# Performance work log

Hardware: AMD Instinct MI355X
Metric: run time of the kernel (lower is better)

Reference implementation:

```python
import jax, jax.numpy as jnp
import numpy as np

BETA = 0.5

def gelu(x):
    return jax.nn.gelu(x, approximate=False)  # torch F.gelu default is exact erf

def setup_inputs() -> dict:
    key = jax.random.key(0)
    ks = jax.random.split(key, 10)
    N, F, PH, P, D, H, C, E = 50000, 128, 64, 8, 4, 128, 10, 1600000
    s = 0.05
    return {
        "x": jax.random.normal(ks[0], (N, F), jnp.float32),
        "W_proj": jax.random.normal(ks[1], (PH, F), jnp.float32) * s,
        "b_proj": jnp.zeros((PH,), jnp.float32),
        "W_x": jax.random.normal(ks[2], (H, F), jnp.float32) * s,
        "b_x": jnp.zeros((H,), jnp.float32),
        "W_path": jax.random.normal(ks[3], (H, D * PH), jnp.float32) * s,
        "b_path": jnp.zeros((H,), jnp.float32),
        "W_A": jax.random.normal(ks[4], (H, N), jnp.float32) * s,
        "b_A": jnp.zeros((H,), jnp.float32),
        "W_end": jax.random.normal(ks[5], (C, H), jnp.float32) * s,
        "b_end": jnp.zeros((C,), jnp.float32),
        "index": jax.random.randint(ks[6], (N, P, D), 0, N, jnp.int64)
                 if jax.config.jax_enable_x64 else jax.random.randint(ks[6], (N, P, D), 0, N, jnp.int32),
        "edge_index": jax.random.randint(ks[7], (2, E), 0, N, jnp.int32),
    }

def reference(x, W_proj, b_proj, W_x, b_x, W_path, b_path, W_A, b_A, W_end, b_end, index, edge_index):
    N = x.shape[0]
    # path projection then per-node path gather: [N, P, D, PH]
    pp = x @ W_proj.T + b_proj
    path = pp[index]
    Np, P, D, PH = path.shape
    # node MLP (dropout off in eval)
    h = gelu(x @ W_x.T + b_x)  # [N, H]
    # concat path encoder: [N, P, D*PH] -> [N, P, H]
    pi = gelu(path.reshape(Np, P, D * PH) @ W_path.T + b_path)
    # dot-product path attention with softmax over path dim
    att = jax.nn.softmax(jnp.einsum('nh,nph->np', h, pi), axis=-1)
    path_agg = jnp.einsum('np,nph->nh', att, pi)
    # sparse adjacency (COO, weights=1) times Linear weight: A @ W_A.T + b_A
    M = W_A.T  # [N, H]
    A_x = jax.ops.segment_sum(M[edge_index[1]], edge_index[0], num_segments=N) + b_A
    out = (1.0 - BETA) * (path_agg + h) + BETA * A_x
    out = gelu(out)
    return out @ W_end.T + b_end
```

## Files before the change

### kernel.cpp

```cpp
#include <hip/hip_runtime.h>
#include <hip/hip_bf16.h>
#include <math.h>

#define NF   128
#define NPH  64
#define NP   8
#define ND   4
#define NH   128
#define NC   10
#define BCAP 2560

typedef __bf16 bf16;
typedef __attribute__((ext_vector_type(4))) __bf16 bf16x4;
typedef __attribute__((ext_vector_type(8))) __bf16 bf16x8;
typedef __attribute__((ext_vector_type(4))) float f32x4;

template<int CTRL>
__device__ __forceinline__ float dpp_add(float x) {
    int t = __builtin_amdgcn_update_dpp(0, __float_as_int(x), CTRL, 0xf, 0xf, false);
    return x + __int_as_float(t);
}
__device__ __forceinline__ float row16_sum(float x) {
    x = dpp_add<0x121>(x);
    x = dpp_add<0x122>(x);
    x = dpp_add<0x124>(x);
    x = dpp_add<0x128>(x);
    return x;
}

__device__ __forceinline__ float gelu_fast(float x) {
    float z = fabsf(x) * 0.70710678118654752f;
    float t = __builtin_amdgcn_rcpf(1.0f + 0.47047f * z);
    float poly = t * (0.3480242f + t * (-0.0958798f + t * 0.7478556f));
    float erfv = 1.0f - poly * __expf(-z * z);
    float s = copysignf(erfv, x);
    return 0.5f * x * (1.0f + s);
}

#define GLOAD_LDS16(g, l)                                                     \
    __builtin_amdgcn_global_load_lds(                                         \
        (const __attribute__((address_space(1))) unsigned int*)(g),           \
        (__attribute__((address_space(3))) unsigned int*)(l), 16, 0, 0)

__device__ __forceinline__ bf16x8 cvt8(float4 a, float4 b) {
    bf16x8 r;
    r[0] = (bf16)a.x; r[1] = (bf16)a.y; r[2] = (bf16)a.z; r[3] = (bf16)a.w;
    r[4] = (bf16)b.x; r[5] = (bf16)b.y; r[6] = (bf16)b.z; r[7] = (bf16)b.w;
    return r;
}

__device__ __forceinline__ void add8(float* a, uint4 v) {
    a[0] += __uint_as_float(v.x << 16);  a[1] += __uint_as_float(v.x & 0xffff0000u);
    a[2] += __uint_as_float(v.y << 16);  a[3] += __uint_as_float(v.y & 0xffff0000u);
    a[4] += __uint_as_float(v.z << 16);  a[5] += __uint_as_float(v.z & 0xffff0000u);
    a[6] += __uint_as_float(v.w << 16);  a[7] += __uint_as_float(v.w & 0xffff0000u);
}

__global__ __launch_bounds__(256) void k_front(
    const float* __restrict__ x,
    const float* __restrict__ Wproj, const float* __restrict__ bproj,
    const float* __restrict__ Wx,    const float* __restrict__ bx,
    bf16* __restrict__ pp, bf16* __restrict__ hb,
    const float* __restrict__ WA, bf16* __restrict__ Mb,
    const int* __restrict__ esrc, const int* __restrict__ edst,
    int* __restrict__ gcur, unsigned* __restrict__ pairs,
    int N, int E, int nbuck, int nbP, int nbT)
{
    __shared__ alignas(16) char smem[33280];
    const int tid = threadIdx.x;

    const int bid = blockIdx.x;
    const int two = 2 * nbP;
    int cls, idx;
    if (bid < two) { cls = bid & 1; idx = bid >> 1; }
    else           { cls = 1; idx = nbP + (bid - two); }

    if (cls == 0) {
        bf16* x_s = (bf16*)smem;
        const int w = tid >> 6, l = tid & 63;
        const int c = l & 15, g = l >> 4;

        bf16x8 bfr[3][4];
        float bias[3];
        #pragma unroll
        for (int t = 0; t < 3; ++t) {
            int ch = (w * 3 + t) * 16 + c;
            const float* wr = (ch < NPH) ? &Wproj[(size_t)ch * NF]
                                         : &Wx[(size_t)(ch - NPH) * NF];
            bias[t] = (ch < NPH) ? bproj[ch] : bx[ch - NPH];
            #pragma unroll
            for (int ks = 0; ks < 4; ++ks) {
                const float* src = wr + ks * 32 + g * 8;
                bfr[t][ks] = cvt8(*(const float4*)src, *(const float4*)(src + 4));
            }
        }

        const int n0 = idx * 64;
        #pragma unroll
        for (int rr = 0; rr < 8; ++rr) {
            int id  = rr * 256 + tid;
            int row = id >> 5, c4 = id & 31;
            float4 v = make_float4(0.f, 0.f, 0.f, 0.f);
            if (n0 + row < N) v = *(const float4*)&x[(size_t)(n0 + row) * NF + c4 * 4];
            bf16x4 o;
            o[0] = (bf16)v.x; o[1] = (bf16)v.y; o[2] = (bf16)v.z; o[3] = (bf16)v.w;
            *(bf16x4*)&x_s[row * 136 + c4 * 4] = o;
        }
        __syncthreads();

        f32x4 acc[4][3] = {};
        #pragma unroll
        for (int rt = 0; rt < 4; ++rt)
            #pragma unroll
            for (int ks = 0; ks < 4; ++ks) {
                bf16x8 a = *(const bf16x8*)&x_s[(rt * 16 + c) * 136 + ks * 32 + g * 8];
                #pragma unroll
                for (int t = 0; t < 3; ++t)
                    acc[rt][t] = __builtin_amdgcn_mfma_f32_16x16x32_bf16(
                        a, bfr[t][ks], acc[rt][t], 0, 0, 0);
            }

        #pragma unroll
        for (int rt = 0; rt < 4; ++rt) {
            #pragma unroll
            for (int t = 0; t < 3; ++t) {
                int ch = (w * 3 + t) * 16 + c;
                #pragma unroll
                for (int i = 0; i < 4; ++i) {
                    int n = n0 + rt * 16 + g * 4 + i;
                    if (n >= N) continue;
                    float v = acc[rt][t][i] + bias[t];
                    if (ch < NPH) pp[(size_t)n * NPH + ch] = (bf16)v;
                    else          hb[(size_t)n * NH + (ch - NPH)] = (bf16)gelu_fast(v);
                }
            }
        }
    } else if (idx < nbT) {
        float* tt = (float*)smem;
        const int n0 = idx * 64;
        const int w = tid >> 6, l = tid & 63;
        #pragma unroll
        for (int rep = 0; rep < 32; ++rep) {
            int hh = rep * 4 + w;
            int n  = n0 + l;
            tt[hh * 65 + l] = (n < N) ? WA[(size_t)hh * N + n] : 0.f;
        }
        __syncthreads();
        #pragma unroll
        for (int rep = 0; rep < 32; ++rep) {
            int n_l = rep * 2 + (tid >> 7);
            int n   = n0 + n_l;
            if (n < N) Mb[(size_t)n * NH + (tid & 127)] = (bf16)tt[(tid & 127) * 65 + n_l];
        }
    } else {
        int* cnt  = (int*)smem;
        int* bofs = cnt + 800;
        const int tile = (idx - nbT) * 4096;
        for (int i = tid; i < nbuck; i += 256) cnt[i] = 0;
        __syncthreads();
        #pragma unroll
        for (int k = 0; k < 16; ++k) {
            int i = tile + k * 256 + tid;
            if (i < E) atomicAdd(&cnt[esrc[i] >> 6], 1);
        }
        __syncthreads();
        for (int i = tid; i < nbuck; i += 256) {
            int c = cnt[i];
            bofs[i] = c ? atomicAdd(&gcur[i], c) : 0;
            cnt[i] = 0;
        }
        __syncthreads();
        #pragma unroll
        for (int k = 0; k < 16; ++k) {
            int i = tile + k * 256 + tid;
            if (i < E) {
                int s = esrc[i], b = s >> 6;
                int r = atomicAdd(&cnt[b], 1);
                pairs[(size_t)b * BCAP + bofs[b] + r] =
                    ((unsigned)(s & 63) << 16) | (unsigned)edst[i];
            }
        }
    }
}

__global__ __launch_bounds__(256, 3) void k_mid2(
    const unsigned* __restrict__ pairs, const int* __restrict__ gcur,
    const bf16* __restrict__ Mb, const float* __restrict__ bA,
    bf16* __restrict__ axbuf2,
    const bf16* __restrict__ pp, const bf16* __restrict__ hb,
    const float* __restrict__ Wpath, const float* __restrict__ bpath,
    const int* __restrict__ index, bf16* __restrict__ aggbuf,
    int N, int E, int nbuck, int nrounds)
{
    __shared__ alignas(16) char smem[35328];
    const int tid = threadIdx.x;

    const int bid = blockIdx.x;
    const int two = 2 * nbuck;
    int cls, idx;
    if (bid < two) { cls = bid & 1; idx = bid >> 1; }
    else           { cls = 0; idx = nbuck + (bid - two); }

    if (cls == 1) {
        int* hist  = (int*)smem;
        int* sc    = hist + 64;
        int* cur   = hist + 128;
        unsigned short* dstl = (unsigned short*)(smem + 768);
        const int b = idx, t = tid;
        const int cnt = gcur[b];
        const unsigned* pb = pairs + (size_t)b * BCAP;

        if (t < 64) hist[t] = 0;
        __syncthreads();
        for (int j = t; j < cnt; j += 256)
            atomicAdd(&hist[pb[j] >> 16], 1);
        __syncthreads();
        if (t < 64) sc[t] = hist[t];
        __syncthreads();
        for (int off = 1; off < 64; off <<= 1) {
            int u = (t < 64 && t >= off) ? sc[t - off] : 0;
            __syncthreads();
            if (t < 64) sc[t] += u;
            __syncthreads();
        }
        if (t < 64) cur[t] = sc[t] - hist[t];
        __syncthreads();
        for (int j = t; j < cnt; j += 256) {
            unsigned p = pb[j];
            int pos = atomicAdd(&cur[p >> 16], 1);
            dstl[pos] = (unsigned short)(p & 0xffffu);
        }
        __syncthreads();

        const int w = t >> 6, l = t & 63;
        const int e = l >> 4, q = l & 15;
        const unsigned short* Mu = (const unsigned short*)Mb;
        const int nb0 = b * 64;
        #pragma unroll 1
        for (int it = 0; it < 16; ++it) {
            const int node = it * 4 + w;
            const int n = nb0 + node;
            const int le = sc[node];
            int j = le - hist[node];
            float acc[8] = {0.f, 0.f, 0.f, 0.f, 0.f, 0.f, 0.f, 0.f};
            for (; j + 32 <= le; j += 32) {
                int d[8];
                #pragma unroll
                for (int k = 0; k < 8; ++k) d[k] = dstl[j + k * 4 + e];
                uint4 v[8];
                #pragma unroll
                for (int k = 0; k < 8; ++k)
                    v[k] = *((const uint4*)(Mu + (size_t)d[k] * NH) + q);
                #pragma unroll
                for (int k = 0; k < 8; ++k) add8(acc, v[k]);
            }
            for (; j + 4 <= le; j += 4) {
                int d0 = dstl[j + e];
                uint4 v0 = *((const uint4*)(Mu + (size_t)d0 * NH) + q);
                add8(acc, v0);
            }
            if (e < le - j) {
                int d0 = dstl[j + e];
                uint4 v0 = *((const uint4*)(Mu + (size_t)d0 * NH) + q);
                add8(acc, v0);
            }
            #pragma unroll
            for (int k = 0; k < 8; ++k) {
                acc[k] += __shfl_xor(acc[k], 16, 64);
                acc[k] += __shfl_xor(acc[k], 32, 64);
            }
            if (l < 16 && n < N) {
                float4 bA0 = *(const float4*)&bA[q * 8];
                float4 bA1 = *(const float4*)&bA[q * 8 + 4];
                bf16x8 o;
                o[0] = (bf16)(0.5f * (acc[0] + bA0.x));
                o[1] = (bf16)(0.5f * (acc[1] + bA0.y));
                o[2] = (bf16)(0.5f * (acc[2] + bA0.z));
                o[3] = (bf16)(0.5f * (acc[3] + bA0.w));
                o[4] = (bf16)(0.5f * (acc[4] + bA1.x));
                o[5] = (bf16)(0.5f * (acc[5] + bA1.y));
                o[6] = (bf16)(0.5f * (acc[6] + bA1.z));
                o[7] = (bf16)(0.5f * (acc[7] + bA1.w));
                *(bf16x8*)&axbuf2[(size_t)n * NH + q * 8] = o;
            }
        }
        return;
    }

    bf16*  path_s = (bf16*)smem;
    bf16*  h_sb   = (bf16*)(smem + 32768);
    float* s_red  = (float*)(smem + 34816);

    const int w   = tid >> 6;
    const int l   = tid & 63;
    const int c   = l & 15;
    const int g   = l >> 4;
    const int nl  = g >> 1;

    bf16x8 bfrag[2][8];
    #pragma unroll
    for (int ht = 0; ht < 2; ++ht) {
        int hg = (w * 2 + ht) * 16 + c;
        #pragma unroll
        for (int ks = 0; ks < 8; ++ks) {
            const float* src = &Wpath[(size_t)hg * 256 + ks * 32 + g * 8];
            bfrag[ht][ks] = cvt8(*(const float4*)src, *(const float4*)(src + 4));
        }
    }
    const float bp0 = bpath[(w * 2 + 0) * 16 + c];
    const float bp1 = bpath[(w * 2 + 1) * 16 + c];

    auto stage = [&](int round, int b) {
        const int n0 = round * 4;
        #pragma unroll
        for (int rr = 0; rr < 4; ++rr) {
            int id  = rr * 256 + tid;
            int row = id >> 5;
            int cc  = id & 31;
            int ls  = cc ^ (row & 7);
            int d   = ls >> 3, q = ls & 7;
            int nn  = row >> 3, p = row & 7;
            int idx2 = index[(size_t)(n0 + nn) * (NP * ND) + p * ND + d];
            GLOAD_LDS16(pp + (size_t)idx2 * NPH + q * 8, &path_s[b * 8192 + id * 8]);
        }
        if (tid < 64) {
            int node = tid >> 4, q = tid & 15;
            GLOAD_LDS16(hb + (size_t)(n0 + node) * NH + q * 8,
                        &h_sb[(b * 4 + node) * 128 + q * 8]);
        }
    };

    int r = idx;
    const int G = gridDim.x - nbuck;
    if (r < nrounds) stage(r, 0);
    int buf = 0;

    for (; r < nrounds; r += G) {
        const int n0 = r * 4;
        __syncthreads();
        if (r + G < nrounds) stage(r + G, buf ^ 1);

        f32x4 acc[2][2] = {};
        #pragma unroll
        for (int rt = 0; rt < 2; ++rt) {
            const int rowbase = buf * 8192 + (rt * 16 + c) * 256;
            #pragma unroll
            for (int ks = 0; ks < 8; ++ks) {
                int chunk = (ks * 4 + g) ^ (c & 7);
                bf16x8 a = *(const bf16x8*)&path_s[rowbase + chunk * 8];
                acc[rt][0] = __builtin_amdgcn_mfma_f32_16x16x32_bf16(
                    a, bfrag[0][ks], acc[rt][0], 0, 0, 0);
                acc[rt][1] = __builtin_amdgcn_mfma_f32_16x16x32_bf16(
                    a, bfrag[1][ks], acc[rt][1], 0, 0, 0);
            }
        }

        float pi[2][2][4];
        #pragma unroll
        for (int rt = 0; rt < 2; ++rt) {
            const float hv0 = (float)h_sb[(buf * 4 + rt * 2 + nl) * 128 + w * 32 + c];
            const float hv1 = (float)h_sb[(buf * 4 + rt * 2 + nl) * 128 + w * 32 + 16 + c];
            float sp[4];
            #pragma unroll
            for (int i = 0; i < 4; ++i) {
                pi[rt][0][i] = gelu_fast(acc[rt][0][i] + bp0);
                pi[rt][1][i] = gelu_fast(acc[rt][1][i] + bp1);
                sp[i] = hv0 * pi[rt][0][i] + hv1 * pi[rt][1][i];
            }
            #pragma unroll
            for (int i = 0; i < 4; ++i) sp[i] = row16_sum(sp[i]);
            float v = (c == 0) ? sp[0] : (c == 1) ? sp[1] : (c == 2) ? sp[2] : sp[3];
            if (c < 4) s_red[w * 32 + rt * 16 + g * 4 + c] = v;
        }

        __builtin_amdgcn_sched_barrier(0);
        asm volatile("s_waitcnt lgkmcnt(0)" ::: "memory");
        __builtin_amdgcn_s_barrier();
        __builtin_amdgcn_sched_barrier(0);

        #pragma unroll
        for (int rt = 0; rt < 2; ++rt) {
            float4 r0 = *(const float4*)&s_red[0 * 32 + rt * 16 + g * 4];
            float4 r1 = *(const float4*)&s_red[1 * 32 + rt * 16 + g * 4];
            float4 r2 = *(const float4*)&s_red[2 * 32 + rt * 16 + g * 4];
            float4 r3 = *(const float4*)&s_red[3 * 32 + rt * 16 + g * 4];
            float st[4];
            st[0] = r0.x + r1.x + r2.x + r3.x;
            st[1] = r0.y + r1.y + r2.y + r3.y;
            st[2] = r0.z + r1.z + r2.z + r3.z;
            st[3] = r0.w + r1.w + r2.w + r3.w;
            float m4 = fmaxf(fmaxf(st[0], st[1]), fmaxf(st[2], st[3]));
            float m  = fmaxf(m4, __shfl_xor(m4, 16, 64));
            float e[4], s4 = 0.f;
            #pragma unroll
            for (int i = 0; i < 4; ++i) { e[i] = __expf(st[i] - m); s4 += e[i]; }
            float den = s4 + __shfl_xor(s4, 16, 64);
            const float inv = __builtin_amdgcn_rcpf(den);

            float pa0 = 0.f, pa1 = 0.f;
            #pragma unroll
            for (int i = 0; i < 4; ++i) {
                pa0 += e[i] * pi[rt][0][i];
                pa1 += e[i] * pi[rt][1][i];
            }
            pa0 = (pa0 + __shfl_xor(pa0, 16, 64)) * inv;
            pa1 = (pa1 + __shfl_xor(pa1, 16, 64)) * inv;

            if (!(g & 1)) {
                int n = n0 + rt * 2 + nl;
                const float hv0 = (float)h_sb[(buf * 4 + rt * 2 + nl) * 128 + w * 32 + c];
                const float hv1 = (float)h_sb[(buf * 4 + rt * 2 + nl) * 128 + w * 32 + 16 + c];
                aggbuf[(size_t)n * NH + w * 32 + c]      = (bf16)(0.5f * (pa0 + hv0));
                aggbuf[(size_t)n * NH + w * 32 + 16 + c] = (bf16)(0.5f * (pa1 + hv1));
            }
        }
        buf ^= 1;
    }
}

__global__ __launch_bounds__(256) void k_fin(
    const bf16* __restrict__ aggbuf, const bf16* __restrict__ axbuf2,
    const float* __restrict__ Wend, const float* __restrict__ bend,
    float* __restrict__ out, int N)
{
    __shared__ float wend_s[NC][128];
    __shared__ float bend_s[NC];
    const int tid = threadIdx.x;
    for (int id = tid; id < NC * 128; id += 256) wend_s[id >> 7][id & 127] = Wend[id];
    if (tid < NC) bend_s[tid] = bend[tid];
    __syncthreads();

    const int w = tid >> 6, l = tid & 63;
    const int n = blockIdx.x * 4 + w;
    if (n >= N) return;
    const int q = l & 15;

    bf16x8 ag = *(const bf16x8*)&aggbuf[(size_t)n * NH + q * 8];
    bf16x8 ax = *(const bf16x8*)&axbuf2[(size_t)n * NH + q * 8];
    float gg[8];
    #pragma unroll
    for (int k = 0; k < 8; ++k)
        gg[k] = gelu_fast((float)ag[k] + (float)ax[k]);

    float part[NC];
    #pragma unroll
    for (int cc = 0; cc < NC; ++cc) {
        float p = 0.f;
        #pragma unroll
        for (int k = 0; k < 8; ++k) p += gg[k] * wend_s[cc][q * 8 + k];
        part[cc] = row16_sum(p);
    }

    float r = part[0];
    #pragma unroll
    for (int cc = 1; cc < NC; ++cc) r = (l == cc) ? part[cc] : r;
    if (l < NC) out[(size_t)n * NC + l] = r + bend_s[l];
}

extern "C" void kernel_launch(void* const* d_in, const int* in_sizes, int n_in,
                              void* d_out, int out_size, void* d_ws, size_t ws_size,
                              hipStream_t stream)
{
    const float* x     = (const float*)d_in[0];
    const float* Wproj = (const float*)d_in[1];
    const float* bproj = (const float*)d_in[2];
    const float* Wx    = (const float*)d_in[3];
    const float* bx    = (const float*)d_in[4];
    const float* Wpath = (const float*)d_in[5];
    const float* bpath = (const float*)d_in[6];
    const float* WA    = (const float*)d_in[7];
    const float* bA    = (const float*)d_in[8];
    const float* Wend  = (const float*)d_in[9];
    const float* bend  = (const float*)d_in[10];
    const int*   index = (const int*)d_in[11];
    const int*   eidx  = (const int*)d_in[12];

    const int N = in_sizes[0] / NF;
    const int E = in_sizes[12] / 2;
    const int* esrc = eidx;
    const int* edst = eidx + E;
    const int nbuck = (N + 63) >> 6;

    char* p = (char*)d_ws;
    auto alloc = [&](size_t bytes) {
        char* r = p;
        p += (bytes + 255) & ~(size_t)255;
        return r;
    };
    bf16*     pp     = (bf16*)alloc((size_t)N * NPH * sizeof(bf16));
    bf16*     hb     = (bf16*)alloc((size_t)N * NH * sizeof(bf16));
    bf16*     aggbuf = (bf16*)alloc((size_t)N * NH * sizeof(bf16));
    bf16*     axbuf2 = (bf16*)alloc((size_t)N * NH * sizeof(bf16));
    bf16*     Mb     = (bf16*)alloc((size_t)N * NH * sizeof(bf16));
    unsigned* pairs  = (unsigned*)alloc((size_t)nbuck * BCAP * sizeof(unsigned));
    int*      gcur   = (int*)alloc((size_t)nbuck * sizeof(int));

    const int nbP = (N + 63) / 64;
    const int nbT = (N + 63) / 64;
    const int nbB = (E + 4095) / 4096;
    const int NPATH = 1024;
    const int nrounds = N / 4;

    hipMemsetAsync(gcur, 0, (size_t)nbuck * sizeof(int), stream);
    k_front<<<nbP + nbT + nbB, 256, 0, stream>>>(
        x, Wproj, bproj, Wx, bx, pp, hb, WA, Mb, esrc, edst, gcur, pairs,
        N, E, nbuck, nbP, nbT);
    k_mid2<<<nbuck + NPATH, 256, 0, stream>>>(
        pairs, gcur, Mb, bA, axbuf2, pp, hb, Wpath, bpath, index, aggbuf,
        N, E, nbuck, nrounds);
    k_fin<<<(N + 3) / 4, 256, 0, stream>>>(aggbuf, axbuf2, Wend, bend,
                                           (float*)d_out, N);
}
```

Measured before the change: 232.0 us.

## Defer softmax epilogue by one round to drop mid-loop barrier

```diff
diff --git a/kernel.cpp b/kernel.cpp
--- a/kernel.cpp
+++ b/kernel.cpp
@@ -192,7 +192,7 @@
     const int* __restrict__ index, bf16* __restrict__ aggbuf,
     int N, int E, int nbuck, int nrounds)
 {
-    __shared__ alignas(16) char smem[35328];
+    __shared__ alignas(16) char smem[35840];
     const int tid = threadIdx.x;
 
     const int bid = blockIdx.x;
@@ -330,60 +330,15 @@
         }
     };
 
-    int r = idx;
-    const int G = gridDim.x - nbuck;
-    if (r < nrounds) stage(r, 0);
-    int buf = 0;
-
-    for (; r < nrounds; r += G) {
-        const int n0 = r * 4;
-        __syncthreads();
-        if (r + G < nrounds) stage(r + G, buf ^ 1);
-
-        f32x4 acc[2][2] = {};
+    auto ep2 = [&](const float pi_p[2][2][4], const float hvs_p[2][2],
+                   int n0_p, int sbp) {
         #pragma unroll
         for (int rt = 0; rt < 2; ++rt) {
-            const int rowbase = buf * 8192 + (rt * 16 + c) * 256;
-            #pragma unroll
-            for (int ks = 0; ks < 8; ++ks) {
-                int chunk = (ks * 4 + g) ^ (c & 7);
-                bf16x8 a = *(const bf16x8*)&path_s[rowbase + chunk * 8];
-                acc[rt][0] = __builtin_amdgcn_mfma_f32_16x16x32_bf16(
-                    a, bfrag[0][ks], acc[rt][0], 0, 0, 0);
-                acc[rt][1] = __builtin_amdgcn_mfma_f32_16x16x32_bf16(
-                    a, bfrag[1][ks], acc[rt][1], 0, 0, 0);
-            }
-        }
-
-        float pi[2][2][4];
-        #pragma unroll
-        for (int rt = 0; rt < 2; ++rt) {
-            const float hv0 = (float)h_sb[(buf * 4 + rt * 2 + nl) * 128 + w * 32 + c];
-            const float hv1 = (float)h_sb[(buf * 4 + rt * 2 + nl) * 128 + w * 32 + 16 + c];
-            float sp[4];
-            #pragma unroll
-            for (int i = 0; i < 4; ++i) {
-                pi[rt][0][i] = gelu_fast(acc[rt][0][i] + bp0);
-                pi[rt][1][i] = gelu_fast(acc[rt][1][i] + bp1);
-                sp[i] = hv0 * pi[rt][0][i] + hv1 * pi[rt][1][i];
-            }
-            #pragma unroll
-            for (int i = 0; i < 4; ++i) sp[i] = row16_sum(sp[i]);
-            float v = (c == 0) ? sp[0] : (c == 1) ? sp[1] : (c == 2) ? sp[2] : sp[3];
-            if (c < 4) s_red[w * 32 + rt * 16 + g * 4 + c] = v;
-        }
-
-        __builtin_amdgcn_sched_barrier(0);
-        asm volatile("s_waitcnt lgkmcnt(0)" ::: "memory");
-        __builtin_amdgcn_s_barrier();
-        __builtin_amdgcn_sched_barrier(0);
-
-        #pragma unroll
-        for (int rt = 0; rt < 2; ++rt) {
-            float4 r0 = *(const float4*)&s_red[0 * 32 + rt * 16 + g * 4];
-            float4 r1 = *(const float4*)&s_red[1 * 32 + rt * 16 + g * 4];
-            float4 r2 = *(const float4*)&s_red[2 * 32 + rt * 16 + g * 4];
-            float4 r3 = *(const float4*)&s_red[3 * 32 + rt * 16 + g * 4];
+            const float* sr = &s_red[sbp * 128];
+            float4 r0 = *(const float4*)&sr[0 * 32 + rt * 16 + g * 4];
+            float4 r1 = *(const float4*)&sr[1 * 32 + rt * 16 + g * 4];
+            float4 r2 = *(const float4*)&sr[2 * 32 + rt * 16 + g * 4];
+            float4 r3 = *(const float4*)&sr[3 * 32 + rt * 16 + g * 4];
             float st[4];
             st[0] = r0.x + r1.x + r2.x + r3.x;
             st[1] = r0.y + r1.y + r2.y + r3.y;
@@ -400,21 +355,78 @@
             float pa0 = 0.f, pa1 = 0.f;
             #pragma unroll
             for (int i = 0; i < 4; ++i) {
-                pa0 += e[i] * pi[rt][0][i];
-                pa1 += e[i] * pi[rt][1][i];
+                pa0 += e[i] * pi_p[rt][0][i];
+                pa1 += e[i] * pi_p[rt][1][i];
             }
             pa0 = (pa0 + __shfl_xor(pa0, 16, 64)) * inv;
             pa1 = (pa1 + __shfl_xor(pa1, 16, 64)) * inv;
 
             if (!(g & 1)) {
-                int n = n0 + rt * 2 + nl;
-                const float hv0 = (float)h_sb[(buf * 4 + rt * 2 + nl) * 128 + w * 32 + c];
-                const float hv1 = (float)h_sb[(buf * 4 + rt * 2 + nl) * 128 + w * 32 + 16 + c];
-                aggbuf[(size_t)n * NH + w * 32 + c]      = (bf16)(0.5f * (pa0 + hv0));
-                aggbuf[(size_t)n * NH + w * 32 + 16 + c] = (bf16)(0.5f * (pa1 + hv1));
-            }
-        }
+                int n = n0_p + rt * 2 + nl;
+                aggbuf[(size_t)n * NH + w * 32 + c]      = (bf16)(0.5f * (pa0 + hvs_p[rt][0]));
+                aggbuf[(size_t)n * NH + w * 32 + 16 + c] = (bf16)(0.5f * (pa1 + hvs_p[rt][1]));
+            }
+        }
+    };
+
+    int r = idx;
+    const int G = gridDim.x - nbuck;
+    if (r < nrounds) stage(r, 0);
+    int buf = 0, sb = 0;
+    float pi_p[2][2][4];
+    float hvs_p[2][2];
+    int n0_p = 0;
+    bool have = false;
+
+    for (; r < nrounds; r += G) {
+        const int n0 = r * 4;
+        __syncthreads();
+        if (r + G < nrounds) stage(r + G, buf ^ 1);
+
+        if (have) ep2(pi_p, hvs_p, n0_p, sb ^ 1);
+
+        f32x4 acc[2][2] = {};
+        #pragma unroll
+        for (int rt = 0; rt < 2; ++rt) {
+            const int rowbase = buf * 8192 + (rt * 16 + c) * 256;
+            #pragma unroll
+            for (int ks = 0; ks < 8; ++ks) {
+                int chunk = (ks * 4 + g) ^ (c & 7);
+                bf16x8 a = *(const bf16x8*)&path_s[rowbase + chunk * 8];
+                acc[rt][0] = __builtin_amdgcn_mfma_f32_16x16x32_bf16(
+                    a, bfrag[0][ks], acc[rt][0], 0, 0, 0);
+                acc[rt][1] = __builtin_amdgcn_mfma_f32_16x16x32_bf16(
+                    a, bfrag[1][ks], acc[rt][1], 0, 0, 0);
+            }
+        }
+
+        #pragma unroll
+        for (int rt = 0; rt < 2; ++rt) {
+            const float hv0 = (float)h_sb[(buf * 4 + rt * 2 + nl) * 128 + w * 32 + c];
+            const float hv1 = (float)h_sb[(buf * 4 + rt * 2 + nl) * 128 + w * 32 + 16 + c];
+            hvs_p[rt][0] = hv0; hvs_p[rt][1] = hv1;
+            float sp[4];
+            #pragma unroll
+            for (int i = 0; i < 4; ++i) {
+                pi_p[rt][0][i] = gelu_fast(acc[rt][0][i] + bp0);
+                pi_p[rt][1][i] = gelu_fast(acc[rt][1][i] + bp1);
+                sp[i] = hv0 * pi_p[rt][0][i] + hv1 * pi_p[rt][1][i];
+            }
+            #pragma unroll
+            for (int i = 0; i < 4; ++i) sp[i] = row16_sum(sp[i]);
+            float v = (c == 0) ? sp[0] : (c == 1) ? sp[1] : (c == 2) ? sp[2] : sp[3];
+            if (c < 4) s_red[sb * 128 + w * 32 + rt * 16 + g * 4 + c] = v;
+        }
+
+        n0_p = n0;
+        have = true;
+        sb ^= 1;
         buf ^= 1;
+    }
+
+    if (have) {
+        __syncthreads();
+        ep2(pi_p, hvs_p, n0_p, sb ^ 1);
     }
 }
 
```

Result: no change. 230.3 us (-0.8%).
